# Optimization experiments

Measured on AMD Instinct MI355X. Metric: run time of the kernel, lower is better.

Reference implementation:

```python
import jax, jax.numpy as jnp
import numpy as np

B, L, C = 2, 1024, 512
H, P = 8, 4
D = C // H
LN_EPS = 1e-5


def setup_inputs() -> dict:
    key = jax.random.key(0)
    ks = jax.random.split(key, 12)
    s = 0.02
    inp = {
        "features": jax.random.normal(ks[0], (B, L, C), jnp.float32),
        "coords": jax.random.normal(ks[1], (B, L, 3), jnp.float32),
        # LayerNorm params
        "ln_g": jnp.ones((C,), jnp.float32),
        "ln_b": jnp.zeros((C,), jnp.float32),
        # scalar q/k/v projections (stored as [in, out])
        "wq": jax.random.normal(ks[2], (C, C), jnp.float32) * s,
        "bq": jnp.zeros((C,), jnp.float32),
        "wk": jax.random.normal(ks[3], (C, C), jnp.float32) * s,
        "bk": jnp.zeros((C,), jnp.float32),
        "wv": jax.random.normal(ks[4], (C, C), jnp.float32) * s,
        "bv": jnp.zeros((C,), jnp.float32),
        # point q/k/v projections: [C, H*P*3]
        "wqp": jax.random.normal(ks[5], (C, H * P * 3), jnp.float32) * s,
        "bqp": jnp.zeros((H * P * 3,), jnp.float32),
        "wkp": jax.random.normal(ks[6], (C, H * P * 3), jnp.float32) * s,
        "bkp": jnp.zeros((H * P * 3,), jnp.float32),
        "wvp": jax.random.normal(ks[7], (C, H * P * 3), jnp.float32) * s,
        "bvp": jnp.zeros((H * P * 3,), jnp.float32),
        # output projection
        "wo": jax.random.normal(ks[8], (C, C), jnp.float32) * s,
        "bo": jnp.zeros((C,), jnp.float32),
        # per-head point scale, init 1/sqrt(P)
        "pscale": jnp.full((H,), 1.0 / np.sqrt(P), jnp.float32),
    }
    return inp


def _layernorm(x, g, b):
    mu = jnp.mean(x, axis=-1, keepdims=True)
    var = jnp.mean((x - mu) ** 2, axis=-1, keepdims=True)
    return (x - mu) * jax.lax.rsqrt(var + LN_EPS) * g + b


def reference(features, coords, ln_g, ln_b, wq, bq, wk, bk, wv, bv,
              wqp, bqp, wkp, bkp, wvp, bvp, wo, bo, pscale):
    b, l, c = features.shape
    h = pscale.shape[0]
    d = c // h
    p = wqp.shape[1] // (h * 3)

    x = _layernorm(features, ln_g, ln_b)

    # scalar heads: [b,h,l,d]
    q_s = (x @ wq + bq).reshape(b, l, h, d).transpose(0, 2, 1, 3)
    k_s = (x @ wk + bk).reshape(b, l, h, d).transpose(0, 2, 1, 3)
    v_s = (x @ wv + bv).reshape(b, l, h, d).transpose(0, 2, 1, 3)

    # point heads: [b,h,l,p,3]
    q_p = (x @ wqp + bqp).reshape(b, l, h, p, 3).transpose(0, 2, 1, 3, 4)
    k_p = (x @ wkp + bkp).reshape(b, l, h, p, 3).transpose(0, 2, 1, 3, 4)

    # scalar logits
    logits_s = jnp.einsum('bhid,bhjd->bhij', q_s, k_s) * (d ** -0.5)

    # point-distance logits: sum_{p,k} ||q - k||^2 = |q|^2 + |k|^2 - 2 q.k
    # (avoids materializing the [b,h,l,l,p,3] difference tensor)
    dot = jnp.einsum('bhipk,bhjpk->bhij', q_p, k_p)
    qsq = jnp.sum(q_p * q_p, axis=(-1, -2))  # [b,h,l]
    ksq = jnp.sum(k_p * k_p, axis=(-1, -2))  # [b,h,l]
    pdist2 = qsq[..., :, None] + ksq[..., None, :] - 2.0 * dot  # [b,h,l,l]

    logits = logits_s - pdist2 * pscale[None, :, None, None]

    attn = jax.nn.softmax(logits, axis=-1)  # dropout is identity in eval

    out_s = jnp.einsum('bhij,bhjd->bhid', attn, v_s)
    out_s = out_s.transpose(0, 2, 1, 3).reshape(b, l, c)

    out = out_s @ wo + bo  # out_dropout is identity in eval
    return out
```

## Files before the change

kernel.cpp:

```cpp
#include <hip/hip_runtime.h>
#include <math.h>

#define BB 2
#define LL 1024
#define CCH 512
#define HH 8
#define LN_EPSF 1e-5f

typedef short s16x8 __attribute__((ext_vector_type(8)));
typedef float fx4 __attribute__((ext_vector_type(4)));


__device__ __forceinline__ unsigned short f2bf(float f) {
  unsigned u = __float_as_uint(f);
  unsigned r = (u + 0x7FFFu + ((u >> 16) & 1u)) >> 16;
  return (unsigned short)r;
}
__device__ __forceinline__ float bf2f(unsigned short h) {
  return __uint_as_float(((unsigned)h) << 16);
}
__device__ __forceinline__ s16x8 ldfrag(const unsigned short* p) {
  int4 t = *(const int4*)p;
  return *(s16x8*)&t;
}
__device__ __forceinline__ float ex2(float x) {
  float r;
  asm("v_exp_f32 %0, %1" : "=v"(r) : "v"(x));
  return r;
}

template <int CTRL>
__device__ __forceinline__ float dpp_mov(float x) {
  return __int_as_float(
      __builtin_amdgcn_update_dpp(0, __float_as_int(x), CTRL, 0xF, 0xF, true));
}
__device__ __forceinline__ float red16_sum(float v) {
  v += dpp_mov<0x121>(v);
  v += dpp_mov<0x122>(v);
  v += dpp_mov<0x124>(v);
  v += dpp_mov<0x128>(v);
  return v;
}
__device__ __forceinline__ float red16_max(float v) {
  v = fmaxf(v, dpp_mov<0x121>(v));
  v = fmaxf(v, dpp_mov<0x122>(v));
  v = fmaxf(v, dpp_mov<0x124>(v));
  v = fmaxf(v, dpp_mov<0x128>(v));
  return v;
}
__device__ __forceinline__ float wave_sum(float v) {
  v = red16_sum(v);
  v += __shfl_xor(v, 16);
  v += __shfl_xor(v, 32);
  return v;
}

__global__ __launch_bounds__(256) void prep(
    const float* __restrict__ f, const float* __restrict__ g,
    const float* __restrict__ bta, unsigned short* __restrict__ xh,
    unsigned short* __restrict__ xl, const float* __restrict__ wq,
    const float* __restrict__ wk, const float* __restrict__ wv,
    const float* __restrict__ wo, const float* __restrict__ wqp,
    const float* __restrict__ wkp, unsigned short* __restrict__ wt_h,
    unsigned short* __restrict__ qt, unsigned short* __restrict__ kt_,
    float* __restrict__ out) {
  __shared__ unsigned short lh[64][68];
  __shared__ float red[8];
  const int tid = threadIdx.x;
  const int bxg = blockIdx.x;
  if (bxg < 2048) {
    const int row = bxg;
    const int wave = tid >> 6, lane = tid & 63;
    const float* fr = f + (size_t)row * CCH;
    float2 v = *(const float2*)&fr[tid * 2];
    float s = wave_sum(v.x + v.y);
    if (lane == 0) red[wave] = s;
    __syncthreads();
    float mu = (red[0] + red[1] + red[2] + red[3]) * (1.0f / CCH);
    float dx = v.x - mu, dy = v.y - mu;
    float sq = wave_sum(dx * dx + dy * dy);
    if (lane == 0) red[4 + wave] = sq;
    __syncthreads();
    float var = (red[4] + red[5] + red[6] + red[7]) * (1.0f / CCH);
    float inv = 1.0f / sqrtf(var + LN_EPSF);
    float2 gg = *(const float2*)&g[tid * 2];
    float2 bb = *(const float2*)&bta[tid * 2];
    float ox = dx * inv * gg.x + bb.x;
    float oy = dy * inv * gg.y + bb.y;
    unsigned short h0 = f2bf(ox), h1 = f2bf(oy);
    ushort2 hv; hv.x = h0; hv.y = h1;
    ushort2 lv; lv.x = f2bf(ox - bf2f(h0)); lv.y = f2bf(oy - bf2f(h1));
    const int k0c = tid * 2;
    size_t addr = ((size_t)((row >> 4) * 16 + (k0c >> 5))) * 512 +
                  (((k0c >> 3) & 3) * 16 + (row & 15)) * 8 + (k0c & 7);
    *(ushort2*)&xh[addr] = hv;
    *(ushort2*)&xl[addr] = lv;
  } else if (bxg < 2336) {
    const int bx = bxg - 2048;
    const float* W;
    int Ncols, rowbase, kt, nt;
    if (bx < 256) {
      int mat = bx >> 6, t = bx & 63;
      kt = t >> 3; nt = t & 7; Ncols = 512;
      if (mat == 0) { W = wq; rowbase = 0; }
      else if (mat == 1) { W = wk; rowbase = 512; }
      else if (mat == 2) { W = wv; rowbase = 1024; }
      else { W = wo; rowbase = 1536; }
    } else {
      int r = bx - 256; int mat = r >> 4; int t = r & 15;
      kt = t >> 1; nt = t & 1; Ncols = 96;
      if (mat == 0) { W = wqp; rowbase = 2048; }
      else { W = wkp; rowbase = 2144; }
    }
    const int k0 = kt * 64, n0 = nt * 64;
    const int c = tid & 63;
#pragma unroll
    for (int ii = 0; ii < 16; ++ii) {
      int r = ii * 4 + (tid >> 6);
      float val = (n0 + c < Ncols) ? W[(size_t)(k0 + r) * Ncols + n0 + c] : 0.f;
      lh[r][c] = f2bf(val);
    }
    __syncthreads();
    const int base_nt = (rowbase >> 4) + (n0 >> 4);
    const int base_kt = (k0 >> 5);
#pragma unroll
    for (int cc = 0; cc < 2; ++cc) {
      int ch = cc * 256 + tid;
      int lane2 = ch & 63, ktl = (ch >> 6) & 1, ntl = ch >> 7;
      int l16c = lane2 & 15, quadc = lane2 >> 4;
      if (n0 + ntl * 16 < Ncols) {
        unsigned short th[8] __attribute__((aligned(16)));
#pragma unroll
        for (int jj = 0; jj < 8; ++jj)
          th[jj] = lh[ktl * 32 + quadc * 8 + jj][ntl * 16 + l16c];
        *(int4*)&wt_h[((size_t)((base_nt + ntl) * 16 + base_kt + ktl)) * 512 +
                      lane2 * 8] = *(int4*)th;
      }
    }
  } else if (bxg < 2400) {
    const int vb2 = bxg - 2336;
    const int4 zero = {0, 0, 0, 0};
    for (int u = tid; u < 32 * 48; u += 256) {
      int t = u / 48, off = (u - t * 48) * 8;
      int gidx = vb2 * 32 + t;
      unsigned short* dst = (gidx < 1024) ? qt : kt_;
      int rem = gidx & 1023;
      int bh = rem >> 6, lt = rem & 63;
      size_t base = ((size_t)(bh * 64 + lt) * 3 + 2) * 512;
      *(int4*)&dst[base + 128 + off] = zero;
    }
  } else {
    const int vb3 = bxg - 2400;
    const float4 zero = {0.f, 0.f, 0.f, 0.f};
    float4* dst = (float4*)(out + (size_t)vb3 * 4096);
#pragma unroll
    for (int i = 0; i < 4; ++i) dst[i * 256 + tid] = zero;
  }
}

template <int MF, int NF, int TERMS>
__device__ __forceinline__ void mfma_core_frag(
    const unsigned short* __restrict__ Ah, const unsigned short* __restrict__ Al,
    const unsigned short* __restrict__ Bt, int mt0, int ntbase, int nt0,
    int ntmax, int ks0, int ks1, fx4 acc[MF][NF]) {
  const int lane = threadIdx.x & 63;
  int bt[NF];
#pragma unroll
  for (int j = 0; j < NF; ++j) {
    int nt = nt0 + j;
    if (nt > ntmax) nt = ntmax;
    bt[j] = ntbase + nt;
  }
#pragma unroll
  for (int i = 0; i < MF; ++i)
#pragma unroll
    for (int j = 0; j < NF; ++j) acc[i][j] = (fx4){0.f, 0.f, 0.f, 0.f};
  for (int ks = ks0; ks < ks1; ++ks) {
    s16x8 ah[MF], al[MF], b[NF];
#pragma unroll
    for (int i = 0; i < MF; ++i) {
      size_t off = ((size_t)((mt0 + i) * 16 + ks)) * 512 + lane * 8;
      ah[i] = ldfrag(&Ah[off]);
      if (TERMS == 2) al[i] = ldfrag(&Al[off]);
    }
#pragma unroll
    for (int j = 0; j < NF; ++j)
      b[j] = ldfrag(&Bt[((size_t)(bt[j] * 16 + ks)) * 512 + lane * 8]);
#pragma unroll
    for (int i = 0; i < MF; ++i)
#pragma unroll
      for (int j = 0; j < NF; ++j) {
        acc[i][j] = __builtin_amdgcn_mfma_f32_16x16x32_bf16(ah[i], b[j], acc[i][j], 0, 0, 0);
        if (TERMS == 2)
          acc[i][j] = __builtin_amdgcn_mfma_f32_16x16x32_bf16(al[i], b[j], acc[i][j], 0, 0, 0);
      }
  }
}

__global__ __launch_bounds__(256, 4) void proj_mfma(
    const unsigned short* __restrict__ xh, const unsigned short* __restrict__ xl,
    const unsigned short* __restrict__ wt_h,
    const float* __restrict__ bq, const float* __restrict__ bk,
    const float* __restrict__ bv, const float* __restrict__ bqp,
    const float* __restrict__ bkp, const float* __restrict__ pscale,
    unsigned short* __restrict__ qt, unsigned short* __restrict__ kt_,
    unsigned short* __restrict__ vth) {
  __shared__ unsigned short vt_lds[64][72];
  const int bx = blockIdx.x;
  const int m0 = blockIdx.y * 64;
  const int tid = threadIdx.x;
  const int wave = __builtin_amdgcn_readfirstlane(tid >> 6);
  const int lane = tid & 63;
  const int quad = lane >> 4, l16 = lane & 15;
  const int mw = m0 + (wave & 1) * 32;
  const int mt0 = mw >> 4;

  if (bx < 16) {
    const bool isq = bx < 8;
    const float* bias = isq ? bq : bk;
    unsigned short* pdst = isq ? qt : kt_;
    const int n0 = (bx & 7) * 64;
    const int nw = n0 + (wave >> 1) * 32;
    fx4 acc[2][2];
    mfma_core_frag<2, 2, 1>(xh, xh, wt_h, mt0, isq ? 0 : 32, nw >> 4, 31, 0, 16, acc);
#pragma unroll
    for (int j = 0; j < 2; ++j) {
      int n = nw + j * 16 + l16;
      int h = n >> 6, d = n & 63;
      float bb = bias[n];
#pragma unroll
      for (int i = 0; i < 2; ++i)
#pragma unroll
        for (int reg = 0; reg < 4; ++reg) {
          int row = mw + i * 16 + quad * 4 + reg;
          int bi = row >> 10, l = row & 1023;
          int bh2 = bi * 8 + h;
          float val = (acc[i][j][reg] + bb) * 0.4246609f;
          size_t tile = ((size_t)(bh2 * 64 + (l >> 4))) * 3 + (d >> 5);
          pdst[tile * 512 + (((d >> 3) & 3) * 16 + (l & 15)) * 8 + (d & 7)] = f2bf(val);
        }
    }
  } else if (bx < 24) {
    const int h = bx - 16;
    const int nw = h * 64 + (wave >> 1) * 32;
    fx4 acc[2][2];
    mfma_core_frag<2, 2, 2>(xh, xl, wt_h, mt0, 64, nw >> 4, 31, 0, 16, acc);
#pragma unroll
    for (int j = 0; j < 2; ++j) {
      int dl = (wave >> 1) * 32 + j * 16 + l16;
      float bb = bv[h * 64 + dl];
#pragma unroll
      for (int i = 0; i < 2; ++i)
#pragma unroll
        for (int reg = 0; reg < 4; ++reg) {
          int lm = (wave & 1) * 32 + i * 16 + quad * 4 + reg;
          vt_lds[lm][dl] = f2bf(acc[i][j][reg] + bb);
        }
    }
    __syncthreads();
    const int b = m0 >> 10, l0 = m0 & 1023;
    const int bh2 = b * 8 + h;
#pragma unroll
    for (int cc = 0; cc < 2; ++cc) {
      int ch = cc * 256 + tid;
      int lane2 = ch & 63, jt = (ch >> 6) & 1, ft = ch >> 7;
      int l16c = lane2 & 15, quadc = lane2 >> 4;
      unsigned short th[8] __attribute__((aligned(16)));
#pragma unroll
      for (int jj = 0; jj < 8; ++jj)
        th[jj] = vt_lds[jt * 32 + quadc * 8 + jj][ft * 16 + l16c];
      size_t tile = ((size_t)(bh2 * 4 + ft)) * 32 + (l0 >> 5) + jt;
      *(int4*)&vth[tile * 512 + lane2 * 8] = *(int4*)th;
    }
  } else {
    const bool isq = bx < 26;
    const float* bias = isq ? bqp : bkp;
    unsigned short* pdst = isq ? qt : kt_;
    const int n0 = (bx & 1) * 64;
    const int nw = n0 + (wave >> 1) * 32;
    fx4 acc[2][2];
    mfma_core_frag<2, 2, 1>(xh, xh, wt_h, mt0, isq ? 128 : 134, nw >> 4, 5, 0, 16, acc);
#pragma unroll
    for (int j = 0; j < 2; ++j) {
      int n = nw + j * 16 + l16;
      bool ok = n < 96;
      int nn = ok ? n : 0;
      int h = nn / 12, c = nn - h * 12;
      float sc = sqrtf(2.8853901f * pscale[h]);
      float bb = bias[nn];
#pragma unroll
      for (int i = 0; i < 2; ++i)
#pragma unroll
        for (int reg = 0; reg < 4; ++reg) {
          int row = mw + i * 16 + quad * 4 + reg;
          int bi = row >> 10, l = row & 1023;
          int bh2 = bi * 8 + h;
          float val = (acc[i][j][reg] + bb) * sc;
          if (ok) {
            int kc = 64 + c;
            size_t tile = ((size_t)(bh2 * 64 + (l >> 4))) * 3 + 2;
            pdst[tile * 512 + (((kc >> 3) & 3) * 16 + (l & 15)) * 8 + (kc & 7)] =
                f2bf(val);
          }
        }
    }
  }
}

__global__ __launch_bounds__(512, 4) void ipa_attn_mfma(
    const unsigned short* __restrict__ qt, const unsigned short* __restrict__ kt_,
    const unsigned short* __restrict__ vth, const unsigned short* __restrict__ wt_h,
    const float* __restrict__ bo, float* __restrict__ out) {
  const int bid = blockIdx.x;
  const int low3 = bid & 7;
  const int slot = bid >> 3;
  const int qtile = slot & 31;
  const int bh = ((slot >> 5) << 3) | low3;
  const int tid = threadIdx.x;
  const int wave = tid >> 6, lane = tid & 63;
  const int quad = lane >> 4, l16 = lane & 15;
  const int mstrip = wave & 1, kq = wave >> 1;
  const int ibase = qtile * 32 + mstrip * 16;

  __shared__ unsigned short pb[8][16][32];
  __shared__ float obuf[8][16][64];
  __shared__ float mred[8][16], lred[8][16];
  __shared__ float qsl[8][16];
  __shared__ float ks_lds[1024];
  __shared__ __align__(16) unsigned short o_fin[32][64];

  s16x8 aq[3];
#pragma unroll
  for (int s = 0; s < 3; ++s)
    aq[s] = ldfrag(&qt[(((size_t)(bh * 64 + (ibase >> 4))) * 3 + s) * 512 + lane * 8]);

  {
    float qp = 0.f;
#pragma unroll
    for (int j = 0; j < 8; ++j) {
      float v = bf2f((unsigned short)aq[2][j]);
      qp += v * v;
    }
    qp += __shfl_xor(qp, 16);
    qp += __shfl_xor(qp, 32);
    qsl[wave][l16] = 0.5f * qp;
  }
  float qs_r[4];
#pragma unroll
  for (int reg = 0; reg < 4; ++reg) qs_r[reg] = qsl[wave][quad * 4 + reg];

#pragma unroll
  for (int i = 0; i < 8; ++i) {
    int t = wave * 8 + i;
    s16x8 kf = ldfrag(&kt_[(((size_t)(bh * 64 + t)) * 3 + 2) * 512 + lane * 8]);
    float s = 0.f;
#pragma unroll
    for (int j = 0; j < 8; ++j) {
      float v = bf2f((unsigned short)kf[j]);
      s += v * v;
    }
    s += __shfl_xor(s, 16);
    s += __shfl_xor(s, 32);
    if (lane < 16) ks_lds[t * 16 + lane] = 0.5f * s;
  }
  __syncthreads();

  fx4 o[4];
#pragma unroll
  for (int f = 0; f < 4; ++f) o[f] = (fx4){0.f, 0.f, 0.f, 0.f};
  float m_r[4], l_r[4];
#pragma unroll
  for (int reg = 0; reg < 4; ++reg) { m_r[reg] = -INFINITY; l_r[reg] = 0.f; }

#pragma unroll 1
  for (int c = 0; c < 8; ++c) {
    const int j0 = kq * 256 + c * 32;
    s16x8 bk[2][3];
#pragma unroll
    for (int f = 0; f < 2; ++f)
#pragma unroll
      for (int s = 0; s < 3; ++s)
        bk[f][s] = ldfrag(
            &kt_[(((size_t)(bh * 64 + (j0 >> 4) + f)) * 3 + s) * 512 + lane * 8]);
    s16x8 bvh[4];
#pragma unroll
    for (int f = 0; f < 4; ++f)
      bvh[f] = ldfrag(
          &vth[(((size_t)(bh * 4 + f)) * 32 + (j0 >> 5)) * 512 + lane * 8]);

    float ks0 = ks_lds[j0 + l16];
    float ks1 = ks_lds[j0 + 16 + l16];

    fx4 sa[2];
    sa[0] = (fx4){0.f, 0.f, 0.f, 0.f};
    sa[1] = (fx4){0.f, 0.f, 0.f, 0.f};
#pragma unroll
    for (int f = 0; f < 2; ++f)
#pragma unroll
      for (int s = 0; s < 3; ++s)
        sa[f] = __builtin_amdgcn_mfma_f32_16x16x32_bf16(aq[s], bk[f][s], sa[f], 0, 0, 0);

#pragma unroll
    for (int reg = 0; reg < 4; ++reg) {
      float z0 = sa[0][reg] - qs_r[reg] - ks0;
      float z1 = sa[1][reg] - qs_r[reg] - ks1;
      float mx = red16_max(fmaxf(z0, z1));
      float mnew = fmaxf(m_r[reg], mx);
      float p0 = ex2(z0 - mnew), p1 = ex2(z1 - mnew);
      float alpha = ex2(m_r[reg] - mnew);
      float psum = red16_sum(p0 + p1);
      l_r[reg] = l_r[reg] * alpha + psum;
      m_r[reg] = mnew;
      o[0][reg] *= alpha; o[1][reg] *= alpha; o[2][reg] *= alpha; o[3][reg] *= alpha;
      pb[wave][quad * 4 + reg][l16] = f2bf(p0);
      pb[wave][quad * 4 + reg][16 + l16] = f2bf(p1);
    }
    s16x8 ap = ldfrag(&pb[wave][l16][quad * 8]);
#pragma unroll
    for (int f = 0; f < 4; ++f)
      o[f] = __builtin_amdgcn_mfma_f32_16x16x32_bf16(ap, bvh[f], o[f], 0, 0, 0);
  }
  if (l16 == 0) {
#pragma unroll
    for (int reg = 0; reg < 4; ++reg) {
      mred[wave][quad * 4 + reg] = m_r[reg];
      lred[wave][quad * 4 + reg] = l_r[reg];
    }
  }
#pragma unroll
  for (int f = 0; f < 4; ++f)
#pragma unroll
    for (int reg = 0; reg < 4; ++reg)
      obuf[wave][quad * 4 + reg][f * 16 + l16] = o[f][reg];
  __syncthreads();
  if (kq == 0) {
#pragma unroll
    for (int f = 0; f < 4; ++f)
#pragma unroll
      for (int reg = 0; reg < 4; ++reg) {
        int row = quad * 4 + reg;
        int d = f * 16 + l16;
        float M = -INFINITY;
#pragma unroll
        for (int p = 0; p < 4; ++p) M = fmaxf(M, mred[wave + p * 2][row]);
        float L = 0.f, val = 0.f;
#pragma unroll
        for (int p = 0; p < 4; ++p) {
          float w = ex2(mred[wave + p * 2][row] - M);
          L += lred[wave + p * 2][row] * w;
          val += obuf[wave + p * 2][row][d] * w;
        }
        val /= L;
        int rowl = wave * 16 + row;
        o_fin[rowl][(((d >> 3) ^ (rowl & 7)) << 3) + (d & 7)] = f2bf(val);
      }
  }
  __syncthreads();

  {
    const int b = bh >> 3, h = bh & 7;
    const size_t m0 = (size_t)b * LL + qtile * 32;
    s16x8 af[2][2];
#pragma unroll
    for (int mi = 0; mi < 2; ++mi)
#pragma unroll
      for (int k2 = 0; k2 < 2; ++k2) {
        int rowa = mi * 16 + l16;
        af[mi][k2] = ldfrag(&o_fin[rowa][(((k2 * 4 + quad) ^ (rowa & 7)) << 3)]);
      }
#pragma unroll
    for (int np = 0; np < 2; ++np) {
      fx4 acc[2][2];
#pragma unroll
      for (int mi = 0; mi < 2; ++mi)
#pragma unroll
        for (int j = 0; j < 2; ++j) acc[mi][j] = (fx4){0.f, 0.f, 0.f, 0.f};
#pragma unroll
      for (int k2 = 0; k2 < 2; ++k2) {
        s16x8 bw[2];
#pragma unroll
        for (int j = 0; j < 2; ++j) {
          int nt = wave * 4 + np * 2 + j;
          bw[j] = ldfrag(
              &wt_h[((size_t)((96 + nt) * 16 + h * 2 + k2)) * 512 + lane * 8]);
        }
#pragma unroll
        for (int mi = 0; mi < 2; ++mi)
#pragma unroll
          for (int j = 0; j < 2; ++j)
            acc[mi][j] = __builtin_amdgcn_mfma_f32_16x16x32_bf16(
                af[mi][k2], bw[j], acc[mi][j], 0, 0, 0);
      }
#pragma unroll
      for (int j = 0; j < 2; ++j) {
        int n = (wave * 4 + np * 2 + j) * 16 + l16;
        float bb = (h == 0) ? bo[n] : 0.f;
#pragma unroll
        for (int mi = 0; mi < 2; ++mi)
#pragma unroll
          for (int reg = 0; reg < 4; ++reg)
            atomicAdd(&out[(m0 + mi * 16 + quad * 4 + reg) * 512 + n],
                      acc[mi][j][reg] + bb);
      }
    }
  }
}

extern "C" void kernel_launch(void* const* d_in, const int* in_sizes, int n_in,
                              void* d_out, int out_size, void* d_ws, size_t ws_size,
                              hipStream_t stream) {
  (void)in_sizes; (void)n_in; (void)out_size; (void)ws_size;
  const float* features = (const float*)d_in[0];
  const float* ln_g = (const float*)d_in[2];
  const float* ln_b = (const float*)d_in[3];
  const float* wq = (const float*)d_in[4];
  const float* bq = (const float*)d_in[5];
  const float* wk = (const float*)d_in[6];
  const float* bk = (const float*)d_in[7];
  const float* wv = (const float*)d_in[8];
  const float* bv = (const float*)d_in[9];
  const float* wqp = (const float*)d_in[10];
  const float* bqp = (const float*)d_in[11];
  const float* wkp = (const float*)d_in[12];
  const float* bkp = (const float*)d_in[13];
  const float* wo = (const float*)d_in[16];
  const float* bo = (const float*)d_in[17];
  const float* pscale = (const float*)d_in[18];
  float* out = (float*)d_out;

  char* cur = (char*)d_ws;
  const size_t NTOK = (size_t)BB * LL;
  unsigned short* xh = (unsigned short*)cur; cur += NTOK * CCH * 2;
  unsigned short* xl = (unsigned short*)cur; cur += NTOK * CCH * 2;
  unsigned short* wt_h = (unsigned short*)cur; cur += (size_t)2240 * 512 * 2;
  unsigned short* qt = (unsigned short*)cur; cur += (size_t)16 * LL * 96 * 2;
  unsigned short* kt_ = (unsigned short*)cur; cur += (size_t)16 * LL * 96 * 2;
  unsigned short* vth = (unsigned short*)cur; cur += (size_t)16 * 64 * LL * 2;

  prep<<<dim3(2656), 256, 0, stream>>>(features, ln_g, ln_b, xh, xl, wq, wk, wv,
                                       wo, wqp, wkp, wt_h, qt, kt_, out);
  proj_mfma<<<dim3(28, 32), 256, 0, stream>>>(xh, xl, wt_h, bq, bk, bv, bqp, bkp,
                                              pscale, qt, kt_, vth);
  ipa_attn_mfma<<<dim3(512), 512, 0, stream>>>(qt, kt_, vth, wt_h, bo, out);
}
```

Before: 163.9 us.

## Split attention into 16-row query tiles with 8-way key split per block

Each attention block now handles one 16-row query tile instead of two, with all 8 waves splitting the 1024 keys into 128-key chunks, and the grid is doubled to 1024 blocks. Per-key squared norms are kept in registers instead of shared memory, which removes one barrier. The P scratch buffer is aliased into the output-merge buffer so LDS use drops, and launch bounds ask for 8 blocks per CU. The cost is an 8-way softmax merge per row, twice as many Wo fragment loads across blocks, and atomic output writes that are spread over more blocks.

```diff
diff --git a/kernel.cpp b/kernel.cpp
--- a/kernel.cpp
+++ b/kernel.cpp
@@ -307,32 +307,32 @@
   }
 }
 
-__global__ __launch_bounds__(512, 4) void ipa_attn_mfma(
+__global__ __launch_bounds__(512, 8) void ipa_attn_mfma(
     const unsigned short* __restrict__ qt, const unsigned short* __restrict__ kt_,
     const unsigned short* __restrict__ vth, const unsigned short* __restrict__ wt_h,
     const float* __restrict__ bo, float* __restrict__ out) {
   const int bid = blockIdx.x;
   const int low3 = bid & 7;
   const int slot = bid >> 3;
-  const int qtile = slot & 31;
-  const int bh = ((slot >> 5) << 3) | low3;
+  const int qtile = slot & 63;
+  const int bh = ((slot >> 6) << 3) | low3;
   const int tid = threadIdx.x;
   const int wave = tid >> 6, lane = tid & 63;
   const int quad = lane >> 4, l16 = lane & 15;
-  const int mstrip = wave & 1, kq = wave >> 1;
-  const int ibase = qtile * 32 + mstrip * 16;
-
-  __shared__ unsigned short pb[8][16][32];
-  __shared__ float obuf[8][16][64];
+  const int kq = wave;
+  const int ibase = qtile * 16;
+
+  __shared__ __align__(16) float obufF[8 * 16 * 66];
   __shared__ float mred[8][16], lred[8][16];
   __shared__ float qsl[8][16];
-  __shared__ float ks_lds[1024];
-  __shared__ __align__(16) unsigned short o_fin[32][64];
+  __shared__ __align__(16) unsigned short o_fin[16][64];
+
+  unsigned short* pbw = (unsigned short*)&obufF[wave * 16 * 66];
 
   s16x8 aq[3];
 #pragma unroll
   for (int s = 0; s < 3; ++s)
-    aq[s] = ldfrag(&qt[(((size_t)(bh * 64 + (ibase >> 4))) * 3 + s) * 512 + lane * 8]);
+    aq[s] = ldfrag(&qt[(((size_t)(bh * 64 + qtile)) * 3 + s) * 512 + lane * 8]);
 
   {
     float qp = 0.f;
@@ -349,10 +349,10 @@
 #pragma unroll
   for (int reg = 0; reg < 4; ++reg) qs_r[reg] = qsl[wave][quad * 4 + reg];
 
+  float ks_r[8];
 #pragma unroll
   for (int i = 0; i < 8; ++i) {
-    int t = wave * 8 + i;
-    s16x8 kf = ldfrag(&kt_[(((size_t)(bh * 64 + t)) * 3 + 2) * 512 + lane * 8]);
+    s16x8 kf = ldfrag(&kt_[(((size_t)(bh * 64 + kq * 8 + i)) * 3 + 2) * 512 + lane * 8]);
     float s = 0.f;
 #pragma unroll
     for (int j = 0; j < 8; ++j) {
@@ -361,9 +361,8 @@
     }
     s += __shfl_xor(s, 16);
     s += __shfl_xor(s, 32);
-    if (lane < 16) ks_lds[t * 16 + lane] = 0.5f * s;
-  }
-  __syncthreads();
+    ks_r[i] = 0.5f * s;
+  }
 
   fx4 o[4];
 #pragma unroll
@@ -373,8 +372,8 @@
   for (int reg = 0; reg < 4; ++reg) { m_r[reg] = -INFINITY; l_r[reg] = 0.f; }
 
 #pragma unroll 1
-  for (int c = 0; c < 8; ++c) {
-    const int j0 = kq * 256 + c * 32;
+  for (int c = 0; c < 4; ++c) {
+    const int j0 = kq * 128 + c * 32;
     s16x8 bk[2][3];
 #pragma unroll
     for (int f = 0; f < 2; ++f)
@@ -388,8 +387,8 @@
       bvh[f] = ldfrag(
           &vth[(((size_t)(bh * 4 + f)) * 32 + (j0 >> 5)) * 512 + lane * 8]);
 
-    float ks0 = ks_lds[j0 + l16];
-    float ks1 = ks_lds[j0 + 16 + l16];
+    float ks0 = ks_r[2 * c];
+    float ks1 = ks_r[2 * c + 1];
 
     fx4 sa[2];
     sa[0] = (fx4){0.f, 0.f, 0.f, 0.f};
@@ -412,10 +411,10 @@
       l_r[reg] = l_r[reg] * alpha + psum;
       m_r[reg] = mnew;
       o[0][reg] *= alpha; o[1][reg] *= alpha; o[2][reg] *= alpha; o[3][reg] *= alpha;
-      pb[wave][quad * 4 + reg][l16] = f2bf(p0);
-      pb[wave][quad * 4 + reg][16 + l16] = f2bf(p1);
-    }
-    s16x8 ap = ldfrag(&pb[wave][l16][quad * 8]);
+      pbw[(quad * 4 + reg) * 40 + l16] = f2bf(p0);
+      pbw[(quad * 4 + reg) * 40 + 16 + l16] = f2bf(p1);
+    }
+    s16x8 ap = ldfrag(&pbw[l16 * 40 + quad * 8]);
 #pragma unroll
     for (int f = 0; f < 4; ++f)
       o[f] = __builtin_amdgcn_mfma_f32_16x16x32_bf16(ap, bvh[f], o[f], 0, 0, 0);
@@ -431,50 +430,45 @@
   for (int f = 0; f < 4; ++f)
 #pragma unroll
     for (int reg = 0; reg < 4; ++reg)
-      obuf[wave][quad * 4 + reg][f * 16 + l16] = o[f][reg];
+      obufF[((size_t)(wave * 16 + quad * 4 + reg)) * 66 + f * 16 + l16] = o[f][reg];
   __syncthreads();
-  if (kq == 0) {
-#pragma unroll
-    for (int f = 0; f < 4; ++f)
-#pragma unroll
-      for (int reg = 0; reg < 4; ++reg) {
-        int row = quad * 4 + reg;
-        int d = f * 16 + l16;
-        float M = -INFINITY;
-#pragma unroll
-        for (int p = 0; p < 4; ++p) M = fmaxf(M, mred[wave + p * 2][row]);
-        float L = 0.f, val = 0.f;
-#pragma unroll
-        for (int p = 0; p < 4; ++p) {
-          float w = ex2(mred[wave + p * 2][row] - M);
-          L += lred[wave + p * 2][row] * w;
-          val += obuf[wave + p * 2][row][d] * w;
-        }
-        val /= L;
-        int rowl = wave * 16 + row;
-        o_fin[rowl][(((d >> 3) ^ (rowl & 7)) << 3) + (d & 7)] = f2bf(val);
+
+  {
+    const int fm = wave >> 1;
+    const int regbase = 2 * (wave & 1);
+#pragma unroll
+    for (int rr = 0; rr < 2; ++rr) {
+      int reg = regbase + rr;
+      int row = quad * 4 + reg;
+      int d = fm * 16 + l16;
+      float M = -INFINITY;
+#pragma unroll
+      for (int p = 0; p < 8; ++p) M = fmaxf(M, mred[p][row]);
+      float L = 0.f, val = 0.f;
+#pragma unroll
+      for (int p = 0; p < 8; ++p) {
+        float w = ex2(mred[p][row] - M);
+        L += lred[p][row] * w;
+        val += obufF[((size_t)(p * 16 + row)) * 66 + d] * w;
       }
+      val /= L;
+      o_fin[row][(((d >> 3) ^ (row & 7)) << 3) + (d & 7)] = f2bf(val);
+    }
   }
   __syncthreads();
 
   {
     const int b = bh >> 3, h = bh & 7;
-    const size_t m0 = (size_t)b * LL + qtile * 32;
-    s16x8 af[2][2];
-#pragma unroll
-    for (int mi = 0; mi < 2; ++mi)
-#pragma unroll
-      for (int k2 = 0; k2 < 2; ++k2) {
-        int rowa = mi * 16 + l16;
-        af[mi][k2] = ldfrag(&o_fin[rowa][(((k2 * 4 + quad) ^ (rowa & 7)) << 3)]);
-      }
+    const size_t m0 = (size_t)b * LL + ibase;
+    s16x8 af[2];
+#pragma unroll
+    for (int k2 = 0; k2 < 2; ++k2)
+      af[k2] = ldfrag(&o_fin[l16][(((k2 * 4 + quad) ^ (l16 & 7)) << 3)]);
 #pragma unroll
     for (int np = 0; np < 2; ++np) {
-      fx4 acc[2][2];
-#pragma unroll
-      for (int mi = 0; mi < 2; ++mi)
-#pragma unroll
-        for (int j = 0; j < 2; ++j) acc[mi][j] = (fx4){0.f, 0.f, 0.f, 0.f};
+      fx4 acc[2];
+      acc[0] = (fx4){0.f, 0.f, 0.f, 0.f};
+      acc[1] = (fx4){0.f, 0.f, 0.f, 0.f};
 #pragma unroll
       for (int k2 = 0; k2 < 2; ++k2) {
         s16x8 bw[2];
@@ -485,22 +479,16 @@
               &wt_h[((size_t)((96 + nt) * 16 + h * 2 + k2)) * 512 + lane * 8]);
         }
 #pragma unroll
-        for (int mi = 0; mi < 2; ++mi)
-#pragma unroll
-          for (int j = 0; j < 2; ++j)
-            acc[mi][j] = __builtin_amdgcn_mfma_f32_16x16x32_bf16(
-                af[mi][k2], bw[j], acc[mi][j], 0, 0, 0);
+        for (int j = 0; j < 2; ++j)
+          acc[j] = __builtin_amdgcn_mfma_f32_16x16x32_bf16(af[k2], bw[j], acc[j], 0, 0, 0);
       }
 #pragma unroll
       for (int j = 0; j < 2; ++j) {
         int n = (wave * 4 + np * 2 + j) * 16 + l16;
         float bb = (h == 0) ? bo[n] : 0.f;
 #pragma unroll
-        for (int mi = 0; mi < 2; ++mi)
-#pragma unroll
-          for (int reg = 0; reg < 4; ++reg)
-            atomicAdd(&out[(m0 + mi * 16 + quad * 4 + reg) * 512 + n],
-                      acc[mi][j][reg] + bb);
+        for (int reg = 0; reg < 4; ++reg)
+          atomicAdd(&out[(m0 + quad * 4 + reg) * 512 + n], acc[j][reg] + bb);
       }
     }
   }
@@ -541,5 +529,5 @@
                                        wo, wqp, wkp, wt_h, qt, kt_, out);
   proj_mfma<<<dim3(28, 32), 256, 0, stream>>>(xh, xl, wt_h, bq, bk, bv, bqp, bkp,
                                               pscale, qt, kt_, vth);
-  ipa_attn_mfma<<<dim3(512), 512, 0, stream>>>(qt, kt_, vth, wt_h, bo, out);
-}
+  ipa_attn_mfma<<<dim3(1024), 512, 0, stream>>>(qt, kt_, vth, wt_h, bo, out);
+}
```

Result: slower. 188.2 us (+14.9%).
